# Performance work log

Hardware: AMD Instinct MI355X
Metric: run time of the kernel (lower is better)

Reference implementation:

```python
import jax, jax.numpy as jnp
import numpy as np
import math

H, D_MODEL, D_C, D_ROPE = 16, 2048, 512, 64
D_HEAD = D_MODEL // H  # 128
D_QK = D_HEAD + D_ROPE  # 192


def precompute_freqs_cis(d_rope, seq_len, base=10000.0):
    # standard RoPE frequencies over pairs -> (seq_len, d_rope//2)
    inv_freq = 1.0 / (base ** (jnp.arange(0, d_rope, 2, dtype=jnp.float32) / d_rope))
    t = jnp.arange(seq_len, dtype=jnp.float32)
    ang = jnp.outer(t, inv_freq)
    return jnp.cos(ang), jnp.sin(ang)


def apply_rotary_emb(x, cos, sin):
    # x: (..., T, d_rope); cos/sin broadcastable (..., T, d_rope//2); interleaved pairs
    x1 = x[..., 0::2]
    x2 = x[..., 1::2]
    r1 = x1 * cos - x2 * sin
    r2 = x1 * sin + x2 * cos
    return jnp.stack([r1, r2], axis=-1).reshape(x.shape)


def setup_inputs() -> dict:
    key = jax.random.key(0)
    ks = jax.random.split(key, 10)
    B, T = 2, 2048
    s = 0.02
    return {
        "query": jax.random.normal(ks[0], (B, T, D_MODEL), jnp.float32),
        "key": jax.random.normal(ks[1], (B, T, D_MODEL), jnp.float32),
        "value": jax.random.normal(ks[2], (B, T, D_MODEL), jnp.float32),
        # weights stored (in_dim, out_dim)
        "W_DKV": jax.random.normal(ks[3], (D_MODEL, D_C), jnp.float32) * s,
        "W_UK": jax.random.normal(ks[4], (D_C, H * D_HEAD), jnp.float32) * s,
        "W_UV": jax.random.normal(ks[5], (D_C, H * D_HEAD), jnp.float32) * s,
        "W_Q": jax.random.normal(ks[6], (D_MODEL, H * D_HEAD), jnp.float32) * s,
        "W_KR": jax.random.normal(ks[7], (D_MODEL, D_ROPE), jnp.float32) * s,
        "W_QR": jax.random.normal(ks[8], (D_MODEL, H * D_ROPE), jnp.float32) * s,
        "W_O": jax.random.normal(ks[9], (H * D_HEAD, D_MODEL), jnp.float32) * s,
    }


def reference(query, key, value, W_DKV, W_UK, W_UV, W_Q, W_KR, W_QR, W_O):
    B, T_q, _ = query.shape
    T_k = key.shape[1]
    # low-rank latent KV compression
    c_kv = key @ W_DKV                                   # (B, Tk, d_c)
    k_nope = (c_kv @ W_UK).reshape(B, T_k, H, D_HEAD).transpose(0, 2, 1, 3)  # bhkd
    v = (c_kv @ W_UV).reshape(B, T_k, H, D_HEAD).transpose(0, 2, 1, 3)       # bhkd
    q_nope = (query @ W_Q).reshape(B, T_q, H, D_HEAD).transpose(0, 2, 1, 3)  # bhqd
    # decoupled RoPE subspace
    k_rope_in = (key @ W_KR)[:, None, :, :]              # (B,1,Tk,d_rope) shared across heads
    q_rope_in = (query @ W_QR).reshape(B, T_q, H, D_ROPE).transpose(0, 2, 1, 3)
    cos_q, sin_q = precompute_freqs_cis(D_ROPE, T_q)
    cos_k, sin_k = precompute_freqs_cis(D_ROPE, T_k)
    q_rope = apply_rotary_emb(q_rope_in, cos_q[None, None], sin_q[None, None])
    k_rope = apply_rotary_emb(k_rope_in, cos_k[None, None], sin_k[None, None])
    k_rope = jnp.broadcast_to(k_rope, (B, H, T_k, D_ROPE))
    # concat content + rope parts
    q = jnp.concatenate([q_nope, q_rope], axis=-1)       # (B,H,Tq,d_qk)
    k = jnp.concatenate([k_nope, k_rope], axis=-1)       # (B,H,Tk,d_qk)
    scores = jnp.einsum('bhqd,bhkd->bhqk', q, k) / math.sqrt(D_QK)
    p_attn = jax.nn.softmax(scores, axis=-1)             # dropout is identity (eval/p=0)
    x = jnp.einsum('bhqk,bhkd->bhqd', p_attn, v)
    x = x.transpose(0, 2, 1, 3).reshape(B, T_q, H * D_HEAD)
    output = x @ W_O
    return output, p_attn
```

## Files before the change

### kernel.cpp

```cpp
#include <hip/hip_runtime.h>
#include <hip/hip_bf16.h>
#include <math.h>

constexpr int B_   = 2;
constexpr int T_   = 2048;
constexpr int DM   = 2048;
constexpr int H_   = 16;
constexpr int DH   = 128;
constexpr int DC   = 512;
constexpr int DR   = 64;
constexpr int DQK  = DH + DR;
constexpr int BT   = B_ * T_;
constexpr int ZBH  = B_ * H_;

typedef __bf16 bf16x8 __attribute__((ext_vector_type(8)));
typedef float  f32x4  __attribute__((ext_vector_type(4)));
typedef unsigned int u32x2 __attribute__((ext_vector_type(2)));
typedef unsigned short u16x4 __attribute__((ext_vector_type(4)));

__device__ __forceinline__ unsigned pk2(float a, float b) {
  __hip_bfloat162 t = __float22bfloat162_rn(make_float2(a, b));
  return *reinterpret_cast<unsigned*>(&t);
}
__device__ __forceinline__ unsigned short bfbits(float v) {
  __hip_bfloat16 t = __float2bfloat16(v);
  return *reinterpret_cast<unsigned short*>(&t);
}

#define WAITVM(N)   asm volatile("s_waitcnt vmcnt(" #N ")" ::: "memory")
#define BARSB() do { __builtin_amdgcn_s_barrier(); __builtin_amdgcn_sched_barrier(0); } while (0)
#define AS1 __attribute__((address_space(1)))
#define AS3 __attribute__((address_space(3)))

__global__ __launch_bounds__(256)
void prep(const float* __restrict__ query, const float* __restrict__ key,
          const float* __restrict__ W_Q, const float* __restrict__ W_QR,
          const float* __restrict__ W_DKV, const float* __restrict__ W_KR,
          const float* __restrict__ W_UK, const float* __restrict__ W_UV,
          const float* __restrict__ W_O,
          __hip_bfloat16* __restrict__ qB, __hip_bfloat16* __restrict__ kB,
          __hip_bfloat16* __restrict__ Wtqall, __hip_bfloat16* __restrict__ Wtkall,
          __hip_bfloat16* __restrict__ Wtkvup, __hip_bfloat16* __restrict__ WtO,
          float* __restrict__ ctab, float* __restrict__ stab) {
  __shared__ float tile[32][33];
  const int blk = blockIdx.x;
  const int tid = threadIdx.x;

  if (blk < 4096) {
    const float* src = (blk < 2048) ? query : key;
    __hip_bfloat16* dst = (blk < 2048) ? qB : kB;
    const long base = (long)(blk & 2047) * 4096;
    #pragma unroll
    for (int c = 0; c < 4; ++c) {
      const long off = base + c * 1024 + tid * 4;
      float4 f = *(const float4*)(src + off);
      u16x4 pk;
      pk[0] = bfbits(f.x); pk[1] = bfbits(f.y); pk[2] = bfbits(f.z); pk[3] = bfbits(f.w);
      *(u16x4*)(dst + off) = pk;
    }
    return;
  }

  int b = blk - 4096;
  const float* W = nullptr; __hip_bfloat16* Wt = nullptr; int K = 2048, N = 2048;
  if (b < 4096)               { W = W_Q;   Wt = Wtqall; }
  else if ((b -= 4096) < 2048){ W = W_QR;  Wt = Wtqall + (size_t)2048 * 2048; N = 1024; }
  else if ((b -= 2048) < 1024){ W = W_DKV; Wt = Wtkall; N = 512; }
  else if ((b -= 1024) < 128) { W = W_KR;  Wt = Wtkall + (size_t)512 * 2048; N = 64; }
  else if ((b -= 128) < 1024) { W = W_UK;  Wt = Wtkvup; K = 512; }
  else if ((b -= 1024) < 1024){ W = W_UV;  Wt = Wtkvup + (size_t)2048 * 512; K = 512; }
  else if ((b -= 1024) < 4096){ W = W_O;   Wt = WtO; }
  else if ((b -= 4096) < 192) {
    float4 z = {0.f, 0.f, 0.f, 0.f};
    *(float4*)((char*)(Wtkall + (size_t)(576 + b) * 2048) + tid * 16) = z;
    return;
  }
  else {
    b -= 192;
    const int i = b * 256 + tid;
    const int t = i >> 5, j = i & 31;
    double inv = pow(10000.0, -(double)j / 32.0);
    double ang = (double)t * inv;
    ctab[i] = (float)cos(ang);
    stab[i] = (float)sin(ang);
    return;
  }
  const int nx = N >> 5;
  const int n0 = (b % nx) << 5, k0 = (b / nx) << 5;
  const int tx = tid & 31, ty = tid >> 5;
  for (int i = ty; i < 32; i += 8)
    tile[i][tx] = W[(long)(k0 + i) * N + n0 + tx];
  __syncthreads();
  for (int i = ty; i < 32; i += 8)
    Wt[(long)(n0 + i) * K + k0 + tx] = __float2bfloat16(tile[tx][i]);
}

template <int MODE>
__device__ __forceinline__
void gemm4w_core(const __hip_bfloat16* __restrict__ A, const __hip_bfloat16* __restrict__ Bt,
                 void* __restrict__ C0, void* __restrict__ C1,
                 int N, int K, int lda,
                 const float* __restrict__ ctab, const float* __restrict__ stab,
                 int bid, int nwg, char* lds) {
  const int gnx = N >> 8;
  const int cpx = nwg >> 3;
  const int swz = (bid & 7) * cpx + (bid >> 3);
  const int n0 = (swz % gnx) << 8;
  const int m0 = (swz / gnx) << 7;

  const int tid  = threadIdx.x;
  const int wc   = tid >> 6;
  const int lane = tid & 63;
  const int rr   = lane & 15;
  const int kq   = lane >> 4;

  const int cs16 = (((tid & 3) ^ ((tid >> 3) & 3)) << 4);
  const int srow = tid >> 2;

  auto stage = [&](int buf, int k0) {
    char* base = lds + buf * 24576;
    #pragma unroll
    for (int c = 0; c < 2; ++c) {
      const char* src = (const char*)A + (((long)(m0 + c * 64 + srow)) * lda + k0) * 2 + cs16;
      __builtin_amdgcn_global_load_lds((const AS1 void*)src,
          (AS3 void*)(base + c * 4096 + tid * 16), 16, 0, 0);
    }
    #pragma unroll
    for (int c = 0; c < 4; ++c) {
      const char* src = (const char*)Bt + (((long)(n0 + c * 64 + srow)) * K + k0) * 2 + cs16;
      __builtin_amdgcn_global_load_lds((const AS1 void*)src,
          (AS3 void*)(base + 8192 + c * 4096 + tid * 16), 16, 0, 0);
    }
  };

  const int g16 = ((kq ^ ((rr >> 1) & 3)) << 4);
  const int aoff0 = rr * 64 + g16;
  const int boff0 = 8192 + (wc * 64 + rr) * 64 + g16;

  f32x4 acc[8][4] = {};

  auto phase = [&](int buf) {
    char* base = lds + buf * 24576;
    bf16x8 a[8], b[4];
    #pragma unroll
    for (int mf = 0; mf < 8; ++mf) a[mf] = *(const bf16x8*)(base + aoff0 + mf * 1024);
    #pragma unroll
    for (int nf = 0; nf < 4; ++nf) b[nf] = *(const bf16x8*)(base + boff0 + nf * 1024);
    __builtin_amdgcn_s_setprio(1);
    #pragma unroll
    for (int mf = 0; mf < 8; ++mf)
      #pragma unroll
      for (int nf = 0; nf < 4; ++nf)
        acc[mf][nf] = __builtin_amdgcn_mfma_f32_16x16x32_bf16(a[mf], b[nf], acc[mf][nf], 0, 0, 0);
    __builtin_amdgcn_s_setprio(0);
  };

  const int NT = K >> 5;
  stage(0, 0); stage(1, 32);
  int cur = 0;
  for (int t = 0; t < NT; ++t) {
    if (t + 1 < NT) WAITVM(6); else WAITVM(0);
    BARSB();
    if (t + 2 < NT) {
      const int b2 = (cur + 2 >= 3) ? cur - 1 : cur + 2;
      stage(b2, (t + 2) << 5);
    }
    phase(cur);
    cur = (cur + 1 >= 3) ? 0 : cur + 1;
  }

  #pragma unroll
  for (int mf = 0; mf < 8; ++mf) {
    #pragma unroll
    for (int nf = 0; nf < 4; ++nf) {
      const int col = n0 + wc * 64 + nf * 16 + rr;
      const int rbase = m0 + mf * 16 + kq * 4;
      if constexpr (MODE == 1) {
        float* C = (float*)C0;
        #pragma unroll
        for (int j = 0; j < 4; ++j)
          __builtin_nontemporal_store(acc[mf][nf][j], &C[(long)(rbase + j) * N + col]);
      } else if constexpr (MODE == 2) {
        __hip_bfloat16* qall = (__hip_bfloat16*)C0;
        if (col < 2048) {
          #pragma unroll
          for (int j = 0; j < 4; ++j)
            qall[(long)(rbase + j) * 3072 + col] = __float2bfloat16(acc[mf][nf][j]);
        } else {
          const int dr = (col - 2048) & 63;
          const int jj = dr >> 1;
          #pragma unroll
          for (int j = 0; j < 4; ++j) {
            const int row = rbase + j;
            const int t = row & (T_ - 1);
            const float c = ctab[t * 32 + jj], s = stab[t * 32 + jj];
            const float v  = acc[mf][nf][j];
            const float pv = __shfl_xor(v, 1);
            const float res = (dr & 1) ? (pv * s + v * c) : (v * c - pv * s);
            qall[(long)row * 3072 + col] = __float2bfloat16(res);
          }
        }
      } else if constexpr (MODE == 3) {
        __hip_bfloat16* ckv = (__hip_bfloat16*)C0;
        __hip_bfloat16* krp = (__hip_bfloat16*)C1;
        if (col < 512) {
          #pragma unroll
          for (int j = 0; j < 4; ++j)
            ckv[(long)(rbase + j) * 512 + col] = __float2bfloat16(acc[mf][nf][j]);
        } else if (col < 576) {
          const int dr = col - 512;
          const int jj = dr >> 1;
          #pragma unroll
          for (int j = 0; j < 4; ++j) {
            const int row = rbase + j;
            const int t = row & (T_ - 1);
            const float c = ctab[t * 32 + jj], s = stab[t * 32 + jj];
            const float v  = acc[mf][nf][j];
            const float pv = __shfl_xor(v, 1);
            const float res = (dr & 1) ? (pv * s + v * c) : (v * c - pv * s);
            krp[(long)row * 64 + dr] = __float2bfloat16(res);
          }
        }
      } else if constexpr (MODE == 4) {
        __hip_bfloat16* knope = (__hip_bfloat16*)C0;
        __hip_bfloat16* vT    = (__hip_bfloat16*)C1;
        if (col < 2048) {
          #pragma unroll
          for (int j = 0; j < 4; ++j)
            knope[(long)(rbase + j) * 2048 + col] = __float2bfloat16(acc[mf][nf][j]);
        } else {
          const int h = (col - 2048) >> 7, d = (col - 2048) & 127;
          const int z = (rbase >> 11) * 16 + h;
          const int t0 = rbase & (T_ - 1);
          u16x4 pk;
          #pragma unroll
          for (int j = 0; j < 4; ++j) pk[j] = bfbits(acc[mf][nf][j]);
          *(u16x4*)((__hip_bfloat16*)vT + ((long)z * DH + d) * T_ + t0) = pk;
        }
      }
    }
  }
}

template <int MODE>
__global__ __launch_bounds__(256, 2)
void gemm_4w(const __hip_bfloat16* __restrict__ A, const __hip_bfloat16* __restrict__ Bt,
             void* __restrict__ C0, void* __restrict__ C1,
             int M, int N, int K, int lda,
             const float* __restrict__ ctab, const float* __restrict__ stab) {
  __shared__ __align__(16) char lds[73728];
  gemm4w_core<MODE>(A, Bt, C0, C1, N, K, lda, ctab, stab,
                    blockIdx.x, (M >> 7) * (N >> 8), lds);
}

__global__ __launch_bounds__(256, 2)
void proj_qk(const __hip_bfloat16* __restrict__ qB, const __hip_bfloat16* __restrict__ kB,
             const __hip_bfloat16* __restrict__ Wtqall, const __hip_bfloat16* __restrict__ Wtkall,
             __hip_bfloat16* __restrict__ q_all, __hip_bfloat16* __restrict__ ckv,
             __hip_bfloat16* __restrict__ kroper,
             const float* __restrict__ ctab, const float* __restrict__ stab) {
  __shared__ __align__(16) char lds[73728];
  if (blockIdx.x < 384)
    gemm4w_core<2>(qB, Wtqall, q_all, nullptr, 3072, 2048, 2048, ctab, stab,
                   blockIdx.x, 384, lds);
  else
    gemm4w_core<3>(kB, Wtkall, ckv, kroper, 768, 2048, 2048, ctab, stab,
                   blockIdx.x - 384, 96, lds);
}

__global__ __launch_bounds__(512, 2)
void gemm_8w_out(const __hip_bfloat16* __restrict__ A, const __hip_bfloat16* __restrict__ Bt,
                 float* __restrict__ C, int M, int N, int K, int lda) {
  const int gnx = N >> 8;
  const int nwg = (M >> 7) * gnx;
  const int cpx = nwg >> 3;
  const int bid = blockIdx.x;
  const int swz = (bid & 7) * cpx + (bid >> 3);
  const int n0 = (swz % gnx) << 8;
  const int m0 = (swz / gnx) << 7;

  __shared__ __align__(16) char lds[147456];

  const int tid  = threadIdx.x;
  const int wv   = tid >> 6;
  const int lane = tid & 63;
  const int wr   = wv >> 2;
  const int wc   = wv & 3;
  const int rr   = lane & 15;
  const int kq   = lane >> 4;

  const int cs16 = (((tid & 3) ^ ((tid >> 3) & 3)) << 4);
  const long arow  = m0 + (tid >> 2);
  const long brow0 = n0 + (tid >> 2);
  const long brow1 = n0 + 128 + (tid >> 2);

  auto stage = [&](int buf, int kh, int k0) {
    char* base = lds + buf * 49152 + kh * 24576;
    const long kk = (long)k0 + kh * 32;
    const char* asrc = (const char*)A + (arow * lda + kk) * 2 + cs16;
    __builtin_amdgcn_global_load_lds((const AS1 void*)asrc,
                                     (AS3 void*)(base + tid * 16), 16, 0, 0);
    const char* bsrc0 = (const char*)Bt + (brow0 * K + kk) * 2 + cs16;
    __builtin_amdgcn_global_load_lds((const AS1 void*)bsrc0,
                                     (AS3 void*)(base + 8192 + tid * 16), 16, 0, 0);
    const char* bsrc1 = (const char*)Bt + (brow1 * K + kk) * 2 + cs16;
    __builtin_amdgcn_global_load_lds((const AS1 void*)bsrc1,
                                     (AS3 void*)(base + 16384 + tid * 16), 16, 0, 0);
  };

  const int g16 = ((kq ^ ((rr >> 1) & 3)) << 4);
  const int aoff0 = (wr * 64 + rr) * 64 + g16;
  const int boff0 = 8192 + (wc * 64 + rr) * 64 + g16;

  f32x4 acc[4][4] = {};

  auto phase = [&](int buf, int kh) {
    char* base = lds + buf * 49152 + kh * 24576;
    bf16x8 a[4], b[4];
    #pragma unroll
    for (int mf = 0; mf < 4; ++mf) a[mf] = *(const bf16x8*)(base + aoff0 + mf * 1024);
    #pragma unroll
    for (int nf = 0; nf < 4; ++nf) b[nf] = *(const bf16x8*)(base + boff0 + nf * 1024);
    __builtin_amdgcn_s_setprio(1);
    #pragma unroll
    for (int mf = 0; mf < 4; ++mf)
      #pragma unroll
      for (int nf = 0; nf < 4; ++nf)
        acc[mf][nf] = __builtin_amdgcn_mfma_f32_16x16x32_bf16(a[mf], b[nf], acc[mf][nf], 0, 0, 0);
    __builtin_amdgcn_s_setprio(0);
  };

  const int NT = K >> 6;
  stage(0, 0, 0); stage(0, 1, 0);
  stage(1, 0, 64); stage(1, 1, 64);
  int cur = 0;
  for (int t = 0; t < NT; ++t) {
    const int b2 = (cur + 2 >= 3) ? cur - 1 : cur + 2;
    if (t + 2 < NT) {
      const int k2 = (t + 2) << 6;
      WAITVM(9);  BARSB();
      stage(b2, 0, k2);
      phase(cur, 0);
      WAITVM(9);  BARSB();
      stage(b2, 1, k2);
      phase(cur, 1);
    } else if (t + 2 == NT) {
      WAITVM(9);  BARSB();  phase(cur, 0);
      WAITVM(6);  BARSB();  phase(cur, 1);
    } else {
      WAITVM(3);  BARSB();  phase(cur, 0);
      WAITVM(0);  BARSB();  phase(cur, 1);
    }
    cur = (cur + 1 >= 3) ? 0 : cur + 1;
  }

  #pragma unroll
  for (int mf = 0; mf < 4; ++mf) {
    #pragma unroll
    for (int nf = 0; nf < 4; ++nf) {
      const int col = n0 + wc * 64 + nf * 16 + rr;
      const int rbase = m0 + wr * 64 + mf * 16 + kq * 4;
      #pragma unroll
      for (int j = 0; j < 4; ++j)
        __builtin_nontemporal_store(acc[mf][nf][j], &C[(long)(rbase + j) * N + col]);
    }
  }
}

__global__ __launch_bounds__(512, 4)
void fused_attn(const __hip_bfloat16* __restrict__ q_all,
                const __hip_bfloat16* __restrict__ knope,
                const __hip_bfloat16* __restrict__ kroper,
                const __hip_bfloat16* __restrict__ vTg,
                float* __restrict__ patt,
                __hip_bfloat16* __restrict__ xplain) {
  constexpr int KT = 64;
  constexpr int NKT = T_ / KT;
  const int bid = blockIdx.x;
  const int swz = (bid & 7) * 64 + (bid >> 3);
  const int z  = swz >> 4;
  const int q0 = (swz & 15) << 7;
  const int b  = z >> 4, h = z & 15;
  const int tid  = threadIdx.x;
  const int wv   = tid >> 6;
  const int lane = tid & 63;
  const int rr   = lane & 15;
  const int kq   = lane >> 4;
  const float scl = 0.0721687836487032f;

  __shared__ __align__(16) char smem[81920];
  char* const lV = smem + 49152;
  char* const lP = smem + 65536;

  const long qrow = (long)(b * T_) + q0 + wv * 16 + rr;
  const __hip_bfloat16* qn = q_all + qrow * 3072 + h * 128;
  const __hip_bfloat16* qr = q_all + qrow * 3072 + 2048 + h * 64;
  bf16x8 qa[6];
  #pragma unroll
  for (int kc = 0; kc < 4; ++kc) qa[kc] = *(const bf16x8*)(qn + kc * 32 + kq * 8);
  #pragma unroll
  for (int kc = 0; kc < 2; ++kc) qa[4 + kc] = *(const bf16x8*)(qr + kc * 32 + kq * 8);

  auto stage_k = [&](char* dst, int kt0) {
    #pragma unroll
    for (int it = 0; it < 3; ++it) {
      const int off = it * 8192 + wv * 1024;
      const int lb  = off + lane * 16;
      const int row = lb / 384, cb = lb % 384;
      const int scb = cb ^ ((row & 7) << 4);
      const long trow = (long)(b * T_) + kt0 + row;
      const char* src = (scb < 256)
          ? (const char*)knope + trow * 4096 + h * 256 + scb
          : (const char*)kroper + trow * 128 + (scb - 256);
      __builtin_amdgcn_global_load_lds((const AS1 void*)src,
          (AS3 void*)(dst + off), 16, 0, 0);
    }
  };
  auto stage_v = [&](int kt0) {
    #pragma unroll
    for (int it = 0; it < 2; ++it) {
      const int off = it * 8192 + wv * 1024;
      const int lb  = off + lane * 16;
      const int row = lb >> 7, cb = lb & 127;
      const int scb = cb ^ ((row & 7) << 4);
      const char* src = (const char*)vTg + ((long)(z * DH + row) * T_ + kt0) * 2 + scb;
      __builtin_amdgcn_global_load_lds((const AS1 void*)src,
          (AS3 void*)(lV + off), 16, 0, 0);
    }
  };

  auto qkt = [&](const char* kb0, f32x4 (&sacc)[4]) {
    __builtin_amdgcn_s_setprio(1);
    #pragma unroll
    for (int kc = 0; kc < 6; ++kc) {
      #pragma unroll
      for (int n = 0; n < 4; ++n) {
        const int krow = n * 16 + rr;
        bf16x8 kb = *(const bf16x8*)(kb0 + krow * 384 +
                                     ((kc * 64 + kq * 16) ^ ((krow & 7) << 4)));
        sacc[n] = __builtin_amdgcn_mfma_f32_16x16x32_bf16(kb, qa[kc], sacc[n], 0, 0, 0);
      }
    }
    __builtin_amdgcn_s_setprio(0);
  };

  float srun = 0.f;

  stage_k(smem, 0);
  stage_k(smem + 24576, KT);
  for (int kt = 0; kt < NKT; ++kt) {
    if (kt + 1 < NKT) WAITVM(3); else WAITVM(0);
    BARSB();
    if (kt + 2 < NKT) {
      const int nb = (kt + 2) % 3;
      stage_k(smem + nb * 24576, (kt + 2) * KT);
    }
    f32x4 sacc[4] = {};
    qkt(smem + (kt % 3) * 24576, sacc);
    float ts = 0.f;
    #pragma unroll
    for (int n = 0; n < 4; ++n)
      #pragma unroll
      for (int r = 0; r < 4; ++r) ts += __expf(sacc[n][r] * scl);
    ts += __shfl_xor(ts, 16);
    ts += __shfl_xor(ts, 32);
    srun += ts;
  }
  const float pis = 1.f / srun;

  stage_k(smem, 0);
  stage_v(0);
  BARSB();

  f32x4 oacc[8] = {};
  const int prow = wv * 16 + rr;
  int cur = 0;
  for (int kt = 0; kt < NKT; ++kt) {
    WAITVM(0);
    BARSB();
    if (kt + 1 < NKT)
      stage_k(smem + (cur ? 0 : 24576), (kt + 1) * KT);
    const char* lK = smem + (cur ? 24576 : 0);
    f32x4 sacc[4] = {};
    qkt(lK, sacc);
    const int kt0 = kt * KT;
    #pragma unroll
    for (int n = 0; n < 4; ++n) {
      f32x4 pv;
      #pragma unroll
      for (int r = 0; r < 4; ++r) pv[r] = __expf(sacc[n][r] * scl) * pis;
      __builtin_nontemporal_store(pv,
          (f32x4*)(patt + ((long)z * T_ + q0 + prow) * T_ + kt0 + n * 16 + kq * 4));
      u32x2 pw; pw[0] = pk2(pv[0], pv[1]); pw[1] = pk2(pv[2], pv[3]);
      *(u32x2*)(lP + prow * 128 + ((n * 32 + kq * 8) ^ ((prow & 7) << 4))) = pw;
    }
    bf16x8 pa[2];
    #pragma unroll
    for (int kc = 0; kc < 2; ++kc)
      pa[kc] = *(const bf16x8*)(lP + prow * 128 + ((kc * 64 + kq * 16) ^ ((prow & 7) << 4)));
    __builtin_amdgcn_s_setprio(1);
    #pragma unroll
    for (int kc = 0; kc < 2; ++kc) {
      #pragma unroll
      for (int n = 0; n < 8; ++n) {
        const int vrow = n * 16 + rr;
        bf16x8 vb = *(const bf16x8*)(lV + vrow * 128 + ((kc * 64 + kq * 16) ^ ((vrow & 7) << 4)));
        oacc[n] = __builtin_amdgcn_mfma_f32_16x16x32_bf16(pa[kc], vb, oacc[n], 0, 0, 0);
      }
    }
    __builtin_amdgcn_s_setprio(0);
    BARSB();
    if (kt + 1 < NKT) stage_v((kt + 1) * KT);
    cur ^= 1;
  }

  #pragma unroll
  for (int n = 0; n < 8; ++n) {
    #pragma unroll
    for (int r = 0; r < 4; ++r) {
      const int q = q0 + wv * 16 + kq * 4 + r;
      xplain[((long)(b * T_ + q)) * DM + h * DH + n * 16 + rr] = __float2bfloat16(oacc[n][r]);
    }
  }
}

extern "C" void kernel_launch(void* const* d_in, const int* in_sizes, int n_in,
                              void* d_out, int out_size, void* d_ws, size_t ws_size,
                              hipStream_t stream) {
  const float* query = (const float*)d_in[0];
  const float* key   = (const float*)d_in[1];
  const float* W_DKV = (const float*)d_in[3];
  const float* W_UK  = (const float*)d_in[4];
  const float* W_UV  = (const float*)d_in[5];
  const float* W_Q   = (const float*)d_in[6];
  const float* W_KR  = (const float*)d_in[7];
  const float* W_QR  = (const float*)d_in[8];
  const float* W_O   = (const float*)d_in[9];

  float* out  = (float*)d_out;
  float* patt = out + (long)BT * DM;

  char* w = (char*)d_ws;
  auto alloc = [&](size_t bytes) { char* p = w; w += (bytes + 255) & ~(size_t)255; return p; };
  __hip_bfloat16* qB     = (__hip_bfloat16*)alloc((size_t)BT * DM * 2);
  __hip_bfloat16* kB     = (__hip_bfloat16*)alloc((size_t)BT * DM * 2);
  __hip_bfloat16* Wtqall = (__hip_bfloat16*)alloc((size_t)3072 * DM * 2);
  __hip_bfloat16* Wtkall = (__hip_bfloat16*)alloc((size_t)768 * DM * 2);
  __hip_bfloat16* Wtkvup = (__hip_bfloat16*)alloc((size_t)4096 * DC * 2);
  __hip_bfloat16* WtO    = (__hip_bfloat16*)alloc((size_t)DM * DM * 2);
  __hip_bfloat16* q_all  = (__hip_bfloat16*)alloc((size_t)BT * 3072 * 2);
  __hip_bfloat16* ckv    = (__hip_bfloat16*)alloc((size_t)BT * 512 * 2);
  __hip_bfloat16* kroper = (__hip_bfloat16*)alloc((size_t)BT * 64 * 2);
  __hip_bfloat16* knope  = (__hip_bfloat16*)alloc((size_t)BT * 2048 * 2);
  __hip_bfloat16* vT     = (__hip_bfloat16*)alloc((size_t)ZBH * DH * T_ * 2);
  __hip_bfloat16* xplain = (__hip_bfloat16*)alloc((size_t)BT * DM * 2);
  float*          ctab   = (float*)alloc((size_t)T_ * 32 * 4);
  float*          stab   = (float*)alloc((size_t)T_ * 32 * 4);

  prep<<<dim3(17984), 256, 0, stream>>>(
      query, key, W_Q, W_QR, W_DKV, W_KR, W_UK, W_UV, W_O,
      qB, kB, Wtqall, Wtkall, Wtkvup, WtO, ctab, stab);

  proj_qk<<<dim3(480), 256, 0, stream>>>(
      qB, kB, Wtqall, Wtkall, q_all, ckv, kroper, ctab, stab);

  gemm_4w<4><<<dim3(512), 256, 0, stream>>>(
      ckv, Wtkvup, knope, vT, BT, 4096, DC, 512, nullptr, nullptr);

  fused_attn<<<dim3(512), 512, 0, stream>>>(
      q_all, knope, kroper, vT, patt, xplain);

  gemm_8w_out<<<dim3(256), 512, 0, stream>>>(
      xplain, WtO, out, BT, DM, DM, DM);
}
```

Before: 384.4 us.

## Double-buffer V tiles and redistribute P through cross-lane permutes instead of LDS

The V tile now gets its own double buffer and is prefetched together with the next K tile. This removes the second barrier per iteration and lets the vmcnt wait stay partial. The P fragments for the PV MFMA are rearranged across lanes with ds_bpermute rather than a store to LDS followed by a reload. The change trades the LDS round-trip and barrier for more bpermute and select instructions, plus extra LDS for the second V buffer.

After: 425.3 us. +10.7%, slower.

```diff
diff --git a/kernel.cpp b/kernel.cpp
--- a/kernel.cpp
+++ b/kernel.cpp
@@ -16,6 +16,7 @@
 typedef __bf16 bf16x8 __attribute__((ext_vector_type(8)));
 typedef float  f32x4  __attribute__((ext_vector_type(4)));
 typedef unsigned int u32x2 __attribute__((ext_vector_type(2)));
+typedef unsigned int u32x4 __attribute__((ext_vector_type(4)));
 typedef unsigned short u16x4 __attribute__((ext_vector_type(4)));
 
 __device__ __forceinline__ unsigned pk2(float a, float b) {
@@ -389,8 +390,6 @@
   const float scl = 0.0721687836487032f;
 
   __shared__ __align__(16) char smem[81920];
-  char* const lV = smem + 49152;
-  char* const lP = smem + 65536;
 
   const long qrow = (long)(b * T_) + q0 + wv * 16 + rr;
   const __hip_bfloat16* qn = q_all + qrow * 3072 + h * 128;
@@ -416,7 +415,7 @@
           (AS3 void*)(dst + off), 16, 0, 0);
     }
   };
-  auto stage_v = [&](int kt0) {
+  auto stage_v = [&](char* dst, int kt0) {
     #pragma unroll
     for (int it = 0; it < 2; ++it) {
       const int off = it * 8192 + wv * 1024;
@@ -425,7 +424,7 @@
       const int scb = cb ^ ((row & 7) << 4);
       const char* src = (const char*)vTg + ((long)(z * DH + row) * T_ + kt0) * 2 + scb;
       __builtin_amdgcn_global_load_lds((const AS1 void*)src,
-          (AS3 void*)(lV + off), 16, 0, 0);
+          (AS3 void*)(dst + off), 16, 0, 0);
     }
   };
 
@@ -469,21 +468,24 @@
   const float pis = 1.f / srun;
 
   stage_k(smem, 0);
-  stage_v(0);
-  BARSB();
+  stage_v(smem + 49152, 0);
 
   f32x4 oacc[8] = {};
   const int prow = wv * 16 + rr;
-  int cur = 0;
+  const int blo  = (rr + ((kq & 1) << 5)) << 2;
   for (int kt = 0; kt < NKT; ++kt) {
-    WAITVM(0);
+    if (kt == 0) WAITVM(0); else WAITVM(4);
     BARSB();
-    if (kt + 1 < NKT)
-      stage_k(smem + (cur ? 0 : 24576), (kt + 1) * KT);
-    const char* lK = smem + (cur ? 24576 : 0);
+    if (kt + 1 < NKT) {
+      stage_k(smem + ((kt + 1) & 1) * 24576, (kt + 1) * KT);
+      stage_v(smem + 49152 + ((kt + 1) & 1) * 16384, (kt + 1) * KT);
+    }
+    const char* lK = smem + (kt & 1) * 24576;
+    const char* lV = smem + 49152 + (kt & 1) * 16384;
     f32x4 sacc[4] = {};
     qkt(lK, sacc);
     const int kt0 = kt * KT;
+    unsigned pw[4][2];
     #pragma unroll
     for (int n = 0; n < 4; ++n) {
       f32x4 pv;
@@ -491,13 +493,22 @@
       for (int r = 0; r < 4; ++r) pv[r] = __expf(sacc[n][r] * scl) * pis;
       __builtin_nontemporal_store(pv,
           (f32x4*)(patt + ((long)z * T_ + q0 + prow) * T_ + kt0 + n * 16 + kq * 4));
-      u32x2 pw; pw[0] = pk2(pv[0], pv[1]); pw[1] = pk2(pv[2], pv[3]);
-      *(u32x2*)(lP + prow * 128 + ((n * 32 + kq * 8) ^ ((prow & 7) << 4))) = pw;
+      pw[n][0] = pk2(pv[0], pv[1]);
+      pw[n][1] = pk2(pv[2], pv[3]);
     }
     bf16x8 pa[2];
     #pragma unroll
-    for (int kc = 0; kc < 2; ++kc)
-      pa[kc] = *(const bf16x8*)(lP + prow * 128 + ((kc * 64 + kq * 16) ^ ((prow & 7) << 4)));
+    for (int kc = 0; kc < 2; ++kc) {
+      u32x4 wd;
+      #pragma unroll
+      for (int wi = 0; wi < 4; ++wi) {
+        const int addr = blo + ((wi >> 1) << 6);
+        const unsigned lo = (unsigned)__builtin_amdgcn_ds_bpermute(addr, (int)pw[2 * kc][wi & 1]);
+        const unsigned hi = (unsigned)__builtin_amdgcn_ds_bpermute(addr, (int)pw[2 * kc + 1][wi & 1]);
+        wd[wi] = (kq >> 1) ? hi : lo;
+      }
+      pa[kc] = __builtin_bit_cast(bf16x8, wd);
+    }
     __builtin_amdgcn_s_setprio(1);
     #pragma unroll
     for (int kc = 0; kc < 2; ++kc) {
@@ -509,9 +520,6 @@
       }
     }
     __builtin_amdgcn_s_setprio(0);
-    BARSB();
-    if (kt + 1 < NKT) stage_v((kt + 1) * KT);
-    cur ^= 1;
   }
 
   #pragma unroll
```
